# Performance work log

Hardware: AMD Instinct MI355X
Metric: run time of the kernel (lower is better)

## Reference

```python
import jax, jax.numpy as jnp
import numpy as np


def _bilinear_sample(fea, x, y):
    # fea: [B,C,H,W]; x,y: [B,D,HW] pixel coords. grid_sample bilinear, zeros padding, align_corners=True
    B, C, H, W = fea.shape
    x0 = jnp.floor(x)
    y0 = jnp.floor(y)
    wx1 = x - x0
    wy1 = y - y0
    flat = fea.reshape(B, C, H * W)

    def corner(xi, yi, w):
        valid = (xi >= 0) & (xi <= W - 1) & (yi >= 0) & (yi <= H - 1)
        idx = jnp.clip(yi, 0, H - 1).astype(jnp.int32) * W + jnp.clip(xi, 0, W - 1).astype(jnp.int32)
        v = jnp.take_along_axis(flat[:, :, None, :], idx[:, None, :, :], axis=3)  # [B,C,D,HW]
        return v * (w * valid)[:, None]

    return (corner(x0, y0, (1 - wx1) * (1 - wy1)) + corner(x0 + 1, y0, wx1 * (1 - wy1))
            + corner(x0, y0 + 1, (1 - wx1) * wy1) + corner(x0 + 1, y0 + 1, wx1 * wy1))


def _build_proj(p):
    # p: [B,2,4,4] -> 4x4 with top 3x4 = K @ [R|t]
    top = jnp.einsum('bij,bjk->bik', p[:, 1, :3, :3], p[:, 0, :3, :4])
    return p[:, 0].at[:, :3, :4].set(top)


def _forward(depth_values, features, proj_matrices, depth_interval, view_weights, CostNum):
    V = features.shape[0]
    ref_fea = features[0]
    B, C, H, W = ref_fea.shape
    # inverse-depth range sampling (per-pixel, CasMVSNet-style)
    inv_d = 1.0 / depth_values[:, 0]                      # [B,H,W]
    itv = depth_interval[:, 0]                            # [B,H,W]
    low = inv_d - (CostNum / 2.0) * itv
    step = (CostNum * itv) / (CostNum - 1)                # (high-low)/(D-1)
    samp = low[:, None] + jnp.arange(CostNum, dtype=inv_d.dtype)[None, :, None, None] * step[:, None]
    depth = (1.0 / samp).reshape(B, CostNum, H * W)       # back to metric depth [B,D,HW]

    ref_inv = jnp.linalg.inv(_build_proj(proj_matrices[:, 0]))
    ys, xs = jnp.meshgrid(jnp.arange(H, dtype=inv_d.dtype), jnp.arange(W, dtype=inv_d.dtype), indexing='ij')
    xyz = jnp.stack([xs.ravel(), ys.ravel(), jnp.ones(H * W, dtype=inv_d.dtype)], 0)  # [3,HW]

    vol = jnp.zeros((B, 1, CostNum, H, W), inv_d.dtype)
    wsum = jnp.full((B, 1, 1, H, W), 1e-5, inv_d.dtype)
    for i in range(1, V):
        proj = jnp.einsum('bij,bjk->bik', _build_proj(proj_matrices[:, i]), ref_inv)
        rot_xyz = jnp.einsum('bij,jn->bin', proj[:, :3, :3], xyz)                     # [B,3,HW]
        pxyz = rot_xyz[:, :, None, :] * depth[:, None] + proj[:, :3, 3][:, :, None, None]
        gx = pxyz[:, 0] / pxyz[:, 2]
        gy = pxyz[:, 1] / pxyz[:, 2]
        warped = _bilinear_sample(features[i], gx, gy).reshape(B, C, CostNum, H, W)
        wv = (warped * ref_fea[:, :, None]).mean(axis=1, keepdims=True)               # [B,1,D,H,W]
        vw = view_weights[:, i - 1][:, None, None]                                    # [B,1,1,H,W]
        vol = vol + wv * vw
        wsum = wsum + vw
    sim = vol / wsum
    # torch broadcasts [B,1,D,H,W] into the [B,C,D,H,W] buffer -> all C channels equal
    return jnp.broadcast_to(sim, (B, C, CostNum, H, W)).reshape(B, C * CostNum, H, W)


def setup_inputs():
    key = jax.random.key(0)
    ks = jax.random.split(key, 4)
    V, B, C, H, W = 5, 2, 32, 256, 320
    features = jax.random.normal(ks[0], (V, B, C, H, W), jnp.float32)
    depth_values = jax.random.uniform(ks[1], (B, 1, H, W), jnp.float32, minval=0.5, maxval=2.0)
    depth_interval = jax.random.uniform(ks[2], (B, 1, H, W), jnp.float32, minval=0.01, maxval=0.03)
    view_weights = jax.random.uniform(ks[3], (B, V - 1, H, W), jnp.float32, minval=0.1, maxval=1.0)
    K = np.array([[300.0, 0.0, W / 2.0], [0.0, 300.0, H / 2.0], [0.0, 0.0, 1.0]], np.float32)
    proj = np.zeros((B, V, 2, 4, 4), np.float32)
    for v in range(V):
        E = np.eye(4, dtype=np.float32)
        E[0, 3] = 0.1 * v  # camera baseline along x
        proj[:, v, 0] = E
        proj[:, v, 1] = np.eye(4, dtype=np.float32)
        proj[:, v, 1, :3, :3] = K
    return {"depth_values": depth_values, "features": features, "proj_matrices": jnp.asarray(proj),
            "depth_interval": depth_interval, "depth_max": 100, "depth_min": 1, "CostNum": 4,
            "view_weights": view_weights}


def reference(depth_values, features, proj_matrices, depth_interval, depth_max, depth_min, CostNum, view_weights):
    # depth_max/depth_min are unused in the per-pixel sampling path of the original helper
    return _forward(depth_values, features, proj_matrices, depth_interval, view_weights, CostNum)
```

## Files before the change

kernel.cpp:

```cpp
#include <hip/hip_runtime.h>

static constexpr int V  = 5;
static constexpr int B  = 2;
static constexpr int C  = 32;
static constexpr int H  = 256;
static constexpr int W  = 320;
static constexpr int CN = 4;
static constexpr int HW = H * W;
static constexpr int CG = 8;
static constexpr int NG = 4;
static constexpr int XT = W / 64;
static constexpr int NBLK = XT * H * B;

static constexpr size_t PARAMS_OFF = 0;

typedef float f32x2 __attribute__((ext_vector_type(2)));
typedef float f32x4 __attribute__((ext_vector_type(4)));

__device__ __forceinline__ f32x2 ld2(const float* p) {
    f32x2 v;
    __builtin_memcpy(&v, p, sizeof(f32x2));
    return v;
}

__global__ void setup_proj_kernel(const float* __restrict__ pm, float* __restrict__ params) {
    int b = threadIdx.x;
    if (b >= B) return;

    float M[V][16];
    for (int v = 0; v < V; ++v) {
        const float* E  = pm + ((size_t)(b * V + v) * 2 + 0) * 16;
        const float* Km = pm + ((size_t)(b * V + v) * 2 + 1) * 16;
        for (int r = 0; r < 3; ++r)
            for (int c = 0; c < 4; ++c) {
                float s = 0.f;
                for (int k = 0; k < 3; ++k) s += Km[r * 4 + k] * E[k * 4 + c];
                M[v][r * 4 + c] = s;
            }
        for (int c = 0; c < 4; ++c) M[v][12 + c] = E[12 + c];
    }

    float A[9], bb[3];
    for (int r = 0; r < 3; ++r) {
        for (int c = 0; c < 3; ++c) A[r * 3 + c] = M[0][r * 4 + c];
        bb[r] = M[0][r * 4 + 3];
    }
    float det = A[0] * (A[4] * A[8] - A[5] * A[7])
              - A[1] * (A[3] * A[8] - A[5] * A[6])
              + A[2] * (A[3] * A[7] - A[4] * A[6]);
    float id = 1.f / det;
    float Ai[9];
    Ai[0] = (A[4] * A[8] - A[5] * A[7]) * id;
    Ai[1] = (A[2] * A[7] - A[1] * A[8]) * id;
    Ai[2] = (A[1] * A[5] - A[2] * A[4]) * id;
    Ai[3] = (A[5] * A[6] - A[3] * A[8]) * id;
    Ai[4] = (A[0] * A[8] - A[2] * A[6]) * id;
    Ai[5] = (A[2] * A[3] - A[0] * A[5]) * id;
    Ai[6] = (A[3] * A[7] - A[4] * A[6]) * id;
    Ai[7] = (A[1] * A[6] - A[0] * A[7]) * id;
    Ai[8] = (A[0] * A[4] - A[1] * A[3]) * id;
    float bi[3];
    for (int r = 0; r < 3; ++r)
        bi[r] = -(Ai[r * 3 + 0] * bb[0] + Ai[r * 3 + 1] * bb[1] + Ai[r * 3 + 2] * bb[2]);

    float Minv[16];
    for (int r = 0; r < 3; ++r) {
        for (int c = 0; c < 3; ++c) Minv[r * 4 + c] = Ai[r * 3 + c];
        Minv[r * 4 + 3] = bi[r];
    }
    Minv[12] = 0.f; Minv[13] = 0.f; Minv[14] = 0.f; Minv[15] = 1.f;

    for (int v = 1; v < V; ++v) {
        float* dst = params + (size_t)(b * (V - 1) + (v - 1)) * 12;
        for (int r = 0; r < 3; ++r)
            for (int c = 0; c < 4; ++c) {
                float s = 0.f;
                for (int k = 0; k < 4; ++k) s += M[v][r * 4 + k] * Minv[k * 4 + c];
                dst[r * 4 + c] = s;
            }
    }
}

__global__ __launch_bounds__(256) void fused_kernel(
    const float* __restrict__ depth_values,
    const float* __restrict__ features,
    const float* __restrict__ depth_interval,
    const float* __restrict__ view_weights,
    const float* __restrict__ params,
    float* __restrict__ out)
{
    const int tid = threadIdx.x;
    const int p   = tid & 63;
    const int g   = tid >> 6;

    const int d   = blockIdx.x;
    const int u   = d >> 3;
    const int r8  = d & 7;
    const int xt  = u % XT;
    const int rid = r8 * 64 + u / XT;
    const int y   = rid & (H - 1);
    const int b   = rid >> 8;

    const int x   = xt * 64 + p;
    const int pix = y * W + x;

    __shared__ float sp4[48];
    __shared__ float stage[NG][1920];
    float* const sredp = &stage[0][0];
    float* const simp  = &stage[0][1024];

    if (tid < 48) sp4[tid] = params[(size_t)b * 48 + tid];
    __syncthreads();

    const float invd = 1.f / depth_values[(size_t)b * HW + pix];
    const float itv  = depth_interval[(size_t)b * HW + pix];
    const float low  = invd - (CN * 0.5f) * itv;
    const float step = (CN * itv) / (float)(CN - 1);
    float dep[CN];
#pragma unroll
    for (int k = 0; k < CN; ++k) dep[k] = 1.f / (low + (float)k * step);

    const float* refp = features + ((size_t)b * C + g * CG) * HW + pix;
    float rf[CG];
#pragma unroll
    for (int c = 0; c < CG; ++c) rf[c] = __builtin_nontemporal_load(refp + (size_t)c * HW);

    const float fx = (float)x, fy = (float)y;

    float volsum[CN] = {0.f, 0.f, 0.f, 0.f};
    float wsum = 1e-5f;

    for (int iv = 0; iv < V - 1; ++iv) {
        const float* spv = &sp4[iv * 12];
        const float rx = spv[0] * fx + spv[1] * fy + spv[2];
        const float ry = spv[4] * fx + spv[5] * fy + spv[6];
        const float rz = spv[8] * fx + spv[9] * fy + spv[10];
        const float tx = spv[3], ty = spv[7], tz = spv[11];

        const float vw = view_weights[((size_t)b * (V - 1) + iv) * HW + pix];
        wsum += vw;
        const float scale = vw * (1.f / (float)C);

        const float* srcg = features + ((size_t)((iv + 1) * B + b) * C + g * CG) * HW;

        int   bx_[CN], y0_[CN];
        float wA0[CN], wB0[CN], wA1[CN], wB1[CN];
#pragma unroll
        for (int k = 0; k < CN; ++k) {
            const float dd = dep[k];
            const float px = rx * dd + tx;
            const float py = ry * dd + ty;
            const float pz = rz * dd + tz;
            const float iz = 1.f / pz;
            const float gx = px * iz;
            const float gy = py * iz;

            const float x0f = floorf(gx), y0f = floorf(gy);
            const float wx1 = gx - x0f, wy1 = gy - y0f;
            const float wx0 = 1.f - wx1, wy0 = 1.f - wy1;
            const int x0 = (int)x0f, y0 = (int)y0f;
            const int x1 = x0 + 1, y1 = y0 + 1;

            const bool vx0 = (x0 >= 0) && (x0 <= W - 1);
            const bool vx1 = (x1 >= 0) && (x1 <= W - 1);
            const bool vy0 = (y0 >= 0) && (y0 <= H - 1);
            const bool vy1 = (y1 >= 0) && (y1 <= H - 1);

            const int bx = min(max(x0, 0), W - 2);
            const int s  = x0 - bx;

            const float w00 = wx0 * wy0 * ((vx0 && vy0) ? scale : 0.f);
            const float w10 = wx1 * wy0 * ((vx1 && vy0) ? scale : 0.f);
            const float w01 = wx0 * wy1 * ((vx0 && vy1) ? scale : 0.f);
            const float w11 = wx1 * wy1 * ((vx1 && vy1) ? scale : 0.f);

            wA0[k] = (s == 0) ? w00 : ((s == -1) ? w10 : 0.f);
            wB0[k] = (s == 0) ? w10 : ((s == 1) ? w00 : 0.f);
            wA1[k] = (s == 0) ? w01 : ((s == -1) ? w11 : 0.f);
            wB1[k] = (s == 0) ? w11 : ((s == 1) ? w01 : 0.f);

            bx_[k] = bx;
            y0_[k] = y0;
        }

        bool okrow = true;
#pragma unroll
        for (int k = 0; k < CN; ++k)
            okrow = okrow && (y0_[k] >= y - 1) && (y0_[k] <= y);

        if (__all(okrow)) {
            int o0[CN];
#pragma unroll
            for (int k = 0; k < CN; ++k)
                o0[k] = (y0_[k] - y + 1) * 320 + bx_[k];

#pragma unroll 1
            for (int cc = 0; cc < CG; cc += 2) {
                __syncthreads();
                {
                    const float* s0 = srcg + (size_t)cc * HW;
#pragma unroll
                    for (int it = 0; it < 8; ++it) {
                        const int idx = it * 64 + p;
                        if (idx < 480) {
                            const int f   = idx << 2;
                            const int chl = (f >= 960) ? 1 : 0;
                            const int rem = f - chl * 960;
                            const int j   = rem / 320;
                            const int col = rem - j * 320;
                            const int row = min(max(y - 1 + j, 0), H - 1);
                            const f32x4 v = *(const f32x4*)(s0 + (size_t)chl * HW + row * W + col);
                            *(f32x4*)&stage[g][f] = v;
                        }
                    }
                }
                __syncthreads();
#pragma unroll
                for (int c2 = 0; c2 < 2; ++c2) {
                    const float rfc = rf[cc + c2];
                    const float* L = &stage[g][c2 * 960];
#pragma unroll
                    for (int k = 0; k < CN; ++k) {
                        const float a0 = L[o0[k]];
                        const float a1 = L[o0[k] + 1];
                        const float b0 = L[o0[k] + 320];
                        const float b1 = L[o0[k] + 321];
                        float t = wA0[k] * a0;
                        t = fmaf(wB0[k], a1, t);
                        t = fmaf(wA1[k], b0, t);
                        t = fmaf(wB1[k], b1, t);
                        volsum[k] = fmaf(rfc, t, volsum[k]);
                    }
                }
            }
        } else {
            int ib0[CN], ib1[CN];
#pragma unroll
            for (int k = 0; k < CN; ++k) {
                const int cy0 = min(max(y0_[k],     0), H - 1);
                const int cy1 = min(max(y0_[k] + 1, 0), H - 1);
                ib0[k] = cy0 * W + bx_[k];
                ib1[k] = cy1 * W + bx_[k];
            }
#pragma unroll 1
            for (int c = 0; c < CG; ++c) {
                const float* fc  = srcg + (size_t)c * HW;
                const float  rfc = rf[c];
#pragma unroll 1
                for (int k = 0; k < CN; ++k) {
                    const f32x2 a   = ld2(fc + ib0[k]);
                    const f32x2 bb2 = ld2(fc + ib1[k]);
                    float t = wA0[k] * a.x;
                    t = fmaf(wB0[k], a.y, t);
                    t = fmaf(wA1[k], bb2.x, t);
                    t = fmaf(wB1[k], bb2.y, t);
                    volsum[k] = fmaf(rfc, t, volsum[k]);
                }
            }
        }
    }

    __syncthreads();
#pragma unroll
    for (int k = 0; k < CN; ++k) sredp[(g * CN + k) * 64 + p] = volsum[k];
    __syncthreads();

    {
        const int k = g;
        const float s = sredp[(0 * CN + k) * 64 + p] + sredp[(1 * CN + k) * 64 + p]
                      + sredp[(2 * CN + k) * 64 + p] + sredp[(3 * CN + k) * 64 + p];
        simp[k * 64 + p] = s * (1.f / wsum);
    }
    __syncthreads();

    {
        const int quad = tid & 15;
        const int pc   = tid >> 4;
        float* op = out + (size_t)b * C * CN * HW + y * W + xt * 64 + quad * 4;
#pragma unroll
        for (int j = 0; j < 8; ++j) {
            const int plane = pc * 8 + j;
            const int k     = plane & 3;
            const f32x4 v   = *(const f32x4*)&simp[k * 64 + quad * 4];
            *(f32x4*)(op + (size_t)plane * HW) = v;
        }
    }
}

extern "C" void kernel_launch(void* const* d_in, const int* in_sizes, int n_in,
                              void* d_out, int out_size, void* d_ws, size_t ws_size,
                              hipStream_t stream) {
    const float* depth_values   = (const float*)d_in[0];
    const float* features       = (const float*)d_in[1];
    const float* proj_matrices  = (const float*)d_in[2];
    const float* depth_interval = (const float*)d_in[3];
    const float* view_weights   = (const float*)d_in[7];
    float* out    = (float*)d_out;
    float* params = (float*)d_ws + PARAMS_OFF;

    setup_proj_kernel<<<1, B, 0, stream>>>(proj_matrices, params);

    fused_kernel<<<NBLK, 256, 0, stream>>>(depth_values, features, depth_interval,
                                           view_weights, params, out);
}
```

Baseline: 278.5 us.

## Double-buffer per-wave LDS staging with async global_load_lds DMA

The block-wide `__syncthreads`-based staging of source-feature rows is replaced. Each wave now issues async `global_load_lds` copies into a private double buffer, one channel ahead, and gates on `vmcnt`/`lgkmcnt` waits instead of block barriers. The next view's first channel is prefetched at the end of each view, including on the fallback gather path. View weights and row offsets are loaded or computed once up front. The aim is to hide global-load latency behind the bilinear FMA work and drop block-level synchronisation, at the cost of relying on hand-counted wait counts that could be wrong if the compiler reorders or inserts other memory ops.

Result: slower. 295.3 us (+6.0%).

```diff
diff --git a/kernel.cpp b/kernel.cpp
--- a/kernel.cpp
+++ b/kernel.cpp
@@ -16,11 +16,18 @@
 
 typedef float f32x2 __attribute__((ext_vector_type(2)));
 typedef float f32x4 __attribute__((ext_vector_type(4)));
+typedef unsigned int u32;
 
 __device__ __forceinline__ f32x2 ld2(const float* p) {
     f32x2 v;
     __builtin_memcpy(&v, p, sizeof(f32x2));
     return v;
+}
+
+__device__ __forceinline__ void dma16(const float* g, float* l) {
+    __builtin_amdgcn_global_load_lds(
+        (const __attribute__((address_space(1))) u32*)g,
+        (__attribute__((address_space(3))) u32*)l, 16, 0, 0);
 }
 
 __global__ void setup_proj_kernel(const float* __restrict__ pm, float* __restrict__ params) {
@@ -105,9 +112,9 @@
     const int pix = y * W + x;
 
     __shared__ float sp4[48];
-    __shared__ float stage[NG][1920];
-    float* const sredp = &stage[0][0];
-    float* const simp  = &stage[0][1024];
+    __shared__ float stage[NG][2][960];
+    float* const sredp = &stage[0][0][0];
+    float* const simp  = &stage[0][0][1024];
 
     if (tid < 48) sp4[tid] = params[(size_t)b * 48 + tid];
     __syncthreads();
@@ -120,15 +127,47 @@
 #pragma unroll
     for (int k = 0; k < CN; ++k) dep[k] = 1.f / (low + (float)k * step);
 
+    float vws[V - 1];
+#pragma unroll
+    for (int i = 0; i < V - 1; ++i)
+        vws[i] = view_weights[((size_t)b * (V - 1) + i) * HW + pix];
+    float wsum = 1e-5f;
+#pragma unroll
+    for (int i = 0; i < V - 1; ++i) wsum += vws[i];
+
     const float* refp = features + ((size_t)b * C + g * CG) * HW + pix;
     float rf[CG];
 #pragma unroll
     for (int c = 0; c < CG; ++c) rf[c] = __builtin_nontemporal_load(refp + (size_t)c * HW);
 
+    const int rc0 = max(y - 1, 0);
+    const int rc2 = min(y + 1, H - 1);
+    int offs[4];
+#pragma unroll
+    for (int it = 0; it < 4; ++it) {
+        const int f   = (it * 64 + p) * 4;
+        const int j   = (f >= 640) ? 2 : ((f >= 320) ? 1 : 0);
+        const int col = f - j * 320;
+        const int row = (j == 0) ? rc0 : ((j == 1) ? y : rc2);
+        offs[it] = row * W + col;
+    }
+
+    const float* srcgv[V - 1];
+#pragma unroll
+    for (int i = 0; i < V - 1; ++i)
+        srcgv[i] = features + ((size_t)((i + 1) * B + b) * C + g * CG) * HW;
+
     const float fx = (float)x, fy = (float)y;
-
     float volsum[CN] = {0.f, 0.f, 0.f, 0.f};
-    float wsum = 1e-5f;
+
+    {
+        const float* gsp = srcgv[0];
+        float* lb = &stage[g][0][0];
+        dma16(gsp + offs[0], lb);
+        dma16(gsp + offs[1], lb + 256);
+        dma16(gsp + offs[2], lb + 512);
+        if (p < 48) dma16(gsp + offs[3], lb + 768);
+    }
 
     for (int iv = 0; iv < V - 1; ++iv) {
         const float* spv = &sp4[iv * 12];
@@ -137,11 +176,7 @@
         const float rz = spv[8] * fx + spv[9] * fy + spv[10];
         const float tx = spv[3], ty = spv[7], tz = spv[11];
 
-        const float vw = view_weights[((size_t)b * (V - 1) + iv) * HW + pix];
-        wsum += vw;
-        const float scale = vw * (1.f / (float)C);
-
-        const float* srcg = features + ((size_t)((iv + 1) * B + b) * C + g * CG) * HW;
+        const float scale = vws[iv] * (1.f / (float)C);
 
         int   bx_[CN], y0_[CN];
         float wA0[CN], wB0[CN], wA1[CN], wB1[CN];
@@ -194,43 +229,38 @@
             for (int k = 0; k < CN; ++k)
                 o0[k] = (y0_[k] - y + 1) * 320 + bx_[k];
 
-#pragma unroll 1
-            for (int cc = 0; cc < CG; cc += 2) {
-                __syncthreads();
-                {
-                    const float* s0 = srcg + (size_t)cc * HW;
-#pragma unroll
-                    for (int it = 0; it < 8; ++it) {
-                        const int idx = it * 64 + p;
-                        if (idx < 480) {
-                            const int f   = idx << 2;
-                            const int chl = (f >= 960) ? 1 : 0;
-                            const int rem = f - chl * 960;
-                            const int j   = rem / 320;
-                            const int col = rem - j * 320;
-                            const int row = min(max(y - 1 + j, 0), H - 1);
-                            const f32x4 v = *(const f32x4*)(s0 + (size_t)chl * HW + row * W + col);
-                            *(f32x4*)&stage[g][f] = v;
-                        }
-                    }
+#pragma unroll
+            for (int ch = 0; ch < CG; ++ch) {
+                const int bi = ch & 1;
+                const bool last = (iv == V - 2) && (ch == CG - 1);
+                if (!last) {
+                    asm volatile("s_waitcnt lgkmcnt(0)" ::: "memory");
+                    __builtin_amdgcn_sched_barrier(0);
+                    const float* gsp = (ch < CG - 1)
+                                     ? srcgv[iv] + (size_t)(ch + 1) * HW
+                                     : srcgv[iv + 1];
+                    float* lb = &stage[g][bi ^ 1][0];
+                    dma16(gsp + offs[0], lb);
+                    dma16(gsp + offs[1], lb + 256);
+                    dma16(gsp + offs[2], lb + 512);
+                    if (p < 48) dma16(gsp + offs[3], lb + 768);
+                    asm volatile("s_waitcnt vmcnt(4)" ::: "memory");
+                } else {
+                    asm volatile("s_waitcnt vmcnt(0)" ::: "memory");
                 }
-                __syncthreads();
-#pragma unroll
-                for (int c2 = 0; c2 < 2; ++c2) {
-                    const float rfc = rf[cc + c2];
-                    const float* L = &stage[g][c2 * 960];
-#pragma unroll
-                    for (int k = 0; k < CN; ++k) {
-                        const float a0 = L[o0[k]];
-                        const float a1 = L[o0[k] + 1];
-                        const float b0 = L[o0[k] + 320];
-                        const float b1 = L[o0[k] + 321];
-                        float t = wA0[k] * a0;
-                        t = fmaf(wB0[k], a1, t);
-                        t = fmaf(wA1[k], b0, t);
-                        t = fmaf(wB1[k], b1, t);
-                        volsum[k] = fmaf(rfc, t, volsum[k]);
-                    }
+                __builtin_amdgcn_sched_barrier(0);
+
+                const float rfc = rf[ch];
+                const float* Lb = &stage[g][bi][0];
+#pragma unroll
+                for (int k = 0; k < CN; ++k) {
+                    const f32x2 a  = ld2(Lb + o0[k]);
+                    const f32x2 b2 = ld2(Lb + o0[k] + 320);
+                    float t = wA0[k] * a.x;
+                    t = fmaf(wB0[k], a.y, t);
+                    t = fmaf(wA1[k], b2.x, t);
+                    t = fmaf(wB1[k], b2.y, t);
+                    volsum[k] = fmaf(rfc, t, volsum[k]);
                 }
             }
         } else {
@@ -242,6 +272,7 @@
                 ib0[k] = cy0 * W + bx_[k];
                 ib1[k] = cy1 * W + bx_[k];
             }
+            const float* srcg = srcgv[iv];
 #pragma unroll 1
             for (int c = 0; c < CG; ++c) {
                 const float* fc  = srcg + (size_t)c * HW;
@@ -257,6 +288,14 @@
                     volsum[k] = fmaf(rfc, t, volsum[k]);
                 }
             }
+            if (iv < V - 2) {
+                const float* gsp = srcgv[iv + 1];
+                float* lb = &stage[g][0][0];
+                dma16(gsp + offs[0], lb);
+                dma16(gsp + offs[1], lb + 256);
+                dma16(gsp + offs[2], lb + 512);
+                if (p < 48) dma16(gsp + offs[3], lb + 768);
+            }
         }
     }
 
```

## Register-prefetch next channel pair into LDS staging and drop block barriers

Applied to the files above, without the earlier changes.

Global loads for the next channel pair, or for the next view's first pair, are now issued into registers while the current pair is consumed from LDS. Because each group's staging slice is private to one wave, the per-iteration block-wide barriers are removed. Staging offsets, source pointers and view weights are hoisted out of the view loop, and LDS bilinear reads use paired float2 loads. This costs more VGPRs, which could lower occupancy, and it relies on wave-level ordering for correctness of the LDS reuse.

After: 326.6 us. 17.3% more time.

```diff
diff --git a/kernel.cpp b/kernel.cpp
--- a/kernel.cpp
+++ b/kernel.cpp
@@ -120,15 +120,44 @@
 #pragma unroll
     for (int k = 0; k < CN; ++k) dep[k] = 1.f / (low + (float)k * step);
 
+    float vws[V - 1];
+#pragma unroll
+    for (int i = 0; i < V - 1; ++i)
+        vws[i] = view_weights[((size_t)b * (V - 1) + i) * HW + pix];
+    float wsum = 1e-5f;
+#pragma unroll
+    for (int i = 0; i < V - 1; ++i) wsum += vws[i];
+
     const float* refp = features + ((size_t)b * C + g * CG) * HW + pix;
     float rf[CG];
 #pragma unroll
     for (int c = 0; c < CG; ++c) rf[c] = __builtin_nontemporal_load(refp + (size_t)c * HW);
 
+    int soff[8];
+#pragma unroll
+    for (int it = 0; it < 8; ++it) {
+        const int slot = it * 64 + p;
+        const int f    = slot * 4;
+        const int chl  = (f >= 960) ? 1 : 0;
+        const int rem  = f - chl * 960;
+        const int j    = rem / 320;
+        const int col  = rem - j * 320;
+        const int row  = min(max(y - 1 + j, 0), H - 1);
+        soff[it] = chl * HW + row * W + col;
+    }
+
+    const float* srcgv[V - 1];
+#pragma unroll
+    for (int i = 0; i < V - 1; ++i)
+        srcgv[i] = features + ((size_t)((i + 1) * B + b) * C + g * CG) * HW;
+
     const float fx = (float)x, fy = (float)y;
-
     float volsum[CN] = {0.f, 0.f, 0.f, 0.f};
-    float wsum = 1e-5f;
+
+    f32x4 R[8];
+#pragma unroll
+    for (int it = 0; it < 8; ++it)
+        if (it < 7 || p < 32) R[it] = *(const f32x4*)(srcgv[0] + soff[it]);
 
     for (int iv = 0; iv < V - 1; ++iv) {
         const float* spv = &sp4[iv * 12];
@@ -137,11 +166,7 @@
         const float rz = spv[8] * fx + spv[9] * fy + spv[10];
         const float tx = spv[3], ty = spv[7], tz = spv[11];
 
-        const float vw = view_weights[((size_t)b * (V - 1) + iv) * HW + pix];
-        wsum += vw;
-        const float scale = vw * (1.f / (float)C);
-
-        const float* srcg = features + ((size_t)((iv + 1) * B + b) * C + g * CG) * HW;
+        const float scale = vws[iv] * (1.f / (float)C);
 
         int   bx_[CN], y0_[CN];
         float wA0[CN], wB0[CN], wA1[CN], wB1[CN];
@@ -194,41 +219,37 @@
             for (int k = 0; k < CN; ++k)
                 o0[k] = (y0_[k] - y + 1) * 320 + bx_[k];
 
-#pragma unroll 1
-            for (int cc = 0; cc < CG; cc += 2) {
-                __syncthreads();
-                {
-                    const float* s0 = srcg + (size_t)cc * HW;
-#pragma unroll
-                    for (int it = 0; it < 8; ++it) {
-                        const int idx = it * 64 + p;
-                        if (idx < 480) {
-                            const int f   = idx << 2;
-                            const int chl = (f >= 960) ? 1 : 0;
-                            const int rem = f - chl * 960;
-                            const int j   = rem / 320;
-                            const int col = rem - j * 320;
-                            const int row = min(max(y - 1 + j, 0), H - 1);
-                            const f32x4 v = *(const f32x4*)(s0 + (size_t)chl * HW + row * W + col);
-                            *(f32x4*)&stage[g][f] = v;
-                        }
-                    }
+#pragma unroll
+            for (int ph = 0; ph < 4; ++ph) {
+#pragma unroll
+                for (int it = 0; it < 8; ++it)
+                    if (it < 7 || p < 32)
+                        *(f32x4*)&stage[g][(it * 64 + p) * 4] = R[it];
+
+                if (ph < 3) {
+                    const float* nsrc = srcgv[iv] + (size_t)(2 * (ph + 1)) * HW;
+#pragma unroll
+                    for (int it = 0; it < 8; ++it)
+                        if (it < 7 || p < 32) R[it] = *(const f32x4*)(nsrc + soff[it]);
+                } else if (iv < V - 2) {
+                    const float* nsrc = srcgv[iv + 1];
+#pragma unroll
+                    for (int it = 0; it < 8; ++it)
+                        if (it < 7 || p < 32) R[it] = *(const f32x4*)(nsrc + soff[it]);
                 }
-                __syncthreads();
+
 #pragma unroll
                 for (int c2 = 0; c2 < 2; ++c2) {
-                    const float rfc = rf[cc + c2];
+                    const float rfc = rf[2 * ph + c2];
                     const float* L = &stage[g][c2 * 960];
 #pragma unroll
                     for (int k = 0; k < CN; ++k) {
-                        const float a0 = L[o0[k]];
-                        const float a1 = L[o0[k] + 1];
-                        const float b0 = L[o0[k] + 320];
-                        const float b1 = L[o0[k] + 321];
-                        float t = wA0[k] * a0;
-                        t = fmaf(wB0[k], a1, t);
-                        t = fmaf(wA1[k], b0, t);
-                        t = fmaf(wB1[k], b1, t);
+                        const f32x2 a  = ld2(L + o0[k]);
+                        const f32x2 b2 = ld2(L + o0[k] + 320);
+                        float t = wA0[k] * a.x;
+                        t = fmaf(wB0[k], a.y, t);
+                        t = fmaf(wA1[k], b2.x, t);
+                        t = fmaf(wB1[k], b2.y, t);
                         volsum[k] = fmaf(rfc, t, volsum[k]);
                     }
                 }
@@ -242,6 +263,7 @@
                 ib0[k] = cy0 * W + bx_[k];
                 ib1[k] = cy1 * W + bx_[k];
             }
+            const float* srcg = srcgv[iv];
 #pragma unroll 1
             for (int c = 0; c < CG; ++c) {
                 const float* fc  = srcg + (size_t)c * HW;
@@ -257,6 +279,11 @@
                     volsum[k] = fmaf(rfc, t, volsum[k]);
                 }
             }
+            if (iv < V - 2) {
+#pragma unroll
+                for (int it = 0; it < 8; ++it)
+                    if (it < 7 || p < 32) R[it] = *(const f32x4*)(srcgv[iv + 1] + soff[it]);
+            }
         }
     }
 
```
